# Performance work log

Hardware: AMD Instinct MI355X
Metric: run time of the kernel (lower is better)

Reference implementation:

```python
import jax, jax.numpy as jnp
import numpy as np
from jax import lax

DIM = 192
HEADS = 6
WIDTH = 256
HEIGHT = 128
BATCH = 2


def _conv1x1(x, w):
    # x: [b,c,h,w], w: [o,c] (1x1 conv, no bias)
    return jnp.einsum('bchw,oc->bohw', x, w)


def setup_inputs() -> dict:
    key = jax.random.key(0)
    ks = jax.random.split(key, 7)
    c = DIM
    std = c ** -0.5
    x = jax.random.normal(ks[0], (BATCH, c, HEIGHT, WIDTH), dtype=jnp.float32)
    rpb_table = 0.02 * jax.random.normal(ks[1], (2 * WIDTH - 1, HEADS), dtype=jnp.float32)
    w_qkv = std * jax.random.normal(ks[2], (3 * c, c), dtype=jnp.float32)
    w_depth = (1.0 / 3.0) * jax.random.normal(ks[3], (3 * c, 1, 3, 3), dtype=jnp.float32)
    w_pre = std * jax.random.normal(ks[4], (c, c), dtype=jnp.float32)
    w_out = std * jax.random.normal(ks[5], (c, c), dtype=jnp.float32)
    w_gate = std * jax.random.normal(ks[6], (c, c), dtype=jnp.float32)
    return {"x": x, "rpb_table": rpb_table, "w_qkv": w_qkv, "w_depth": w_depth,
            "w_pre": w_pre, "w_out": w_out, "w_gate": w_gate, "num_heads": HEADS}


def reference(x, rpb_table, w_qkv, w_depth, w_pre, w_out, w_gate, num_heads):
    b, c, h, w = x.shape
    hd = c // num_heads
    scale = hd ** -0.5

    x_gate = jax.nn.silu(_conv1x1(x, w_gate))

    t = _conv1x1(x, w_qkv)  # [b, 3c, h, w]
    qkv = lax.conv_general_dilated(
        t, w_depth, window_strides=(1, 1), padding='SAME',
        feature_group_count=3 * c,
        dimension_numbers=('NCHW', 'OIHW', 'NCHW'))
    q, k, v = jnp.split(qkv, 3, axis=1)

    def _rows(z):
        # 'b (head c) h w -> b h head w c'
        return z.reshape(b, num_heads, hd, h, w).transpose(0, 3, 1, 4, 2)

    q = _rows(q) * scale
    k = _rows(k)
    v = _rows(v)

    attn = jnp.einsum('bhnic,bhnjc->bhnij', q, k)  # [b, h, heads, w, w]

    # relative position bias: index[i, j] = i - j + (w - 1)
    idx = jnp.arange(w)[:, None] - jnp.arange(w)[None, :] + (w - 1)
    bias = rpb_table[idx].transpose(2, 0, 1)  # [heads, w, w]
    attn = jax.nn.softmax(attn + bias[None, None], axis=-1)

    out = jnp.einsum('bhnij,bhnjc->bhnic', attn, v)
    # 'b h head w c -> b (head c) h w'
    out = out.transpose(0, 2, 4, 1, 3).reshape(b, c, h, w)

    out = _conv1x1(out, w_pre) * x_gate
    return _conv1x1(out, w_out)
```

## Files before the change

kernel.cpp:

```cpp
#include <hip/hip_runtime.h>
#include <hip/hip_bf16.h>
#include <math.h>

#define BATCH 2
#define C 192
#define H 128
#define W 256
#define HEADS 6
#define HD 32
#define HW (H * W)
#define C3 (3 * C)
#define NPX (BATCH * HW)

typedef unsigned short ushort_t;
using bf16x8 = __attribute__((ext_vector_type(8))) short;
using f32x4  = __attribute__((ext_vector_type(4))) float;

static __device__ __forceinline__ float bfbits2f(ushort_t u) {
    return __uint_as_float(((unsigned)u) << 16);
}
static __device__ __forceinline__ ushort_t f2bfbits(float f) {
    __hip_bfloat16 h = __float2bfloat16(f);
    return *reinterpret_cast<ushort_t*>(&h);
}

__global__ __launch_bounds__(256) void prep_w_kernel(
    const float* __restrict__ wq, const float* __restrict__ wg,
    const float* __restrict__ wp, const float* __restrict__ wo,
    ushort_t* __restrict__ dst)
{
    const int i = blockIdx.x * 256 + threadIdx.x;
    const float* src; int off, base;
    if (i < 27648)      { src = wq; off = i;         base = 0; }
    else if (i < 36864) { src = wg; off = i - 27648; base = 110592; }
    else if (i < 46080) { src = wp; off = i - 36864; base = 147456; }
    else                { src = wo; off = i - 46080; base = 184320; }
    float4 v = ((const float4*)src)[off];
    if (i < 9216) {
        const float sc = 0.25503488f;
        v.x *= sc; v.y *= sc; v.z *= sc; v.w *= sc;
    }
    ushort4 o;
    o.x = f2bfbits(v.x); o.y = f2bfbits(v.y);
    o.z = f2bfbits(v.z); o.w = f2bfbits(v.w);
    *(ushort4*)(dst + base + off * 4) = o;
}

__global__ __launch_bounds__(256) void transpose_x_kernel(
    const float* __restrict__ x, ushort_t* __restrict__ xt)
{
    __shared__ uint Xs[64 * 97];
    const int p0 = blockIdx.x * 64;
    const int b  = p0 >> 15, hw0 = p0 & (HW - 1);
    const int t  = threadIdx.x;

    {
        const int px = t & 63, g = t >> 6;
        const float* xb = x + (size_t)b * C * HW + hw0 + px;
#pragma unroll
        for (int i = 0; i < 24; ++i) {
            const int cp = g + i * 4;
            const float v0 = xb[(size_t)(2 * cp) * HW];
            const float v1 = xb[(size_t)(2 * cp + 1) * HW];
            Xs[px * 97 + cp] = (uint)f2bfbits(v0) | ((uint)f2bfbits(v1) << 16);
        }
    }
    __syncthreads();
    {
        const int px = t >> 2, grp = t & 3;
        uint* dst = (uint*)(xt + (size_t)(p0 + px) * C) + grp * 24;
        const uint* s = &Xs[px * 97 + grp * 24];
#pragma unroll
        for (int i = 0; i < 6; ++i) {
            uint4 u;
            u.x = s[i * 4 + 0]; u.y = s[i * 4 + 1];
            u.z = s[i * 4 + 2]; u.w = s[i * 4 + 3];
            *(uint4*)(dst + i * 4) = u;
        }
    }
}

template <int MODE, int OUTKIND, int MT>
__global__ __launch_bounds__(256, 2) void conv_mfma_kernel(
    const ushort_t* __restrict__ in_t, const ushort_t* __restrict__ w_bf,
    void* __restrict__ outp, ushort_t* __restrict__ gate, int ostride)
{
    const int lin = blockIdx.x;
    const int xcd = lin & 7;
    const int jj  = lin >> 3;
    const int pin = jj / MT;
    const int m   = jj - pin * MT;
    const int m0  = m * 64;
    const int p0  = (xcd * 32 + pin) * 256;

    const int t  = threadIdx.x;
    const int wv = t >> 6, lane = t & 63, quad = lane >> 4, l16 = lane & 15;

    __shared__ ushort_t smem[18432];
    ushort_t* As = smem;

    const ushort_t* bp = in_t + (size_t)(p0 + wv * 64 + l16) * C + quad * 8;
    bf16x8 bF[6][4];
#pragma unroll
    for (int ks = 0; ks < 6; ++ks)
#pragma unroll
        for (int ct = 0; ct < 4; ++ct)
            bF[ks][ct] = *(const bf16x8*)(bp + (size_t)(ct * 16) * C + ks * 32);

    {
        const int row = t >> 2, cg = (t & 3) * 48;
        const ushort_t* src = w_bf + (size_t)(m0 + row) * C + cg;
        ushort_t* dst = &As[row * 200 + cg];
#pragma unroll
        for (int i = 0; i < 6; ++i)
            *(bf16x8*)(dst + i * 8) = *(const bf16x8*)(src + i * 8);
    }
    __syncthreads();

    f32x4 acc[4][4];
#pragma unroll
    for (int rt = 0; rt < 4; ++rt)
#pragma unroll
        for (int ct = 0; ct < 4; ++ct) acc[rt][ct] = f32x4{0.f, 0.f, 0.f, 0.f};

#pragma unroll
    for (int ks = 0; ks < 6; ++ks) {
        bf16x8 aF[4];
#pragma unroll
        for (int rt = 0; rt < 4; ++rt)
            aF[rt] = *(const bf16x8*)&As[(rt * 16 + l16) * 200 + quad * 8 + ks * 32];
#pragma unroll
        for (int rt = 0; rt < 4; ++rt)
#pragma unroll
            for (int ct = 0; ct < 4; ++ct)
                acc[rt][ct] = __builtin_amdgcn_mfma_f32_16x16x32_bf16(
                    aF[rt], bF[ks][ct], acc[rt][ct], 0, 0, 0);
    }

    const bool isg = (MODE == 3) && (m >= 9);
    if (MODE == 1 || isg) {
#pragma unroll
        for (int rt = 0; rt < 4; ++rt)
#pragma unroll
            for (int ct = 0; ct < 4; ++ct) {
                f32x4 v = acc[rt][ct];
#pragma unroll
                for (int r = 0; r < 4; ++r)
                    v[r] = v[r] / (1.f + __expf(-v[r]));
                acc[rt][ct] = v;
            }
    }
    if (MODE == 2) {
#pragma unroll
        for (int rt = 0; rt < 4; ++rt)
#pragma unroll
            for (int ct = 0; ct < 4; ++ct) {
                const int px = p0 + wv * 64 + ct * 16 + l16;
                const int ch = m0 + rt * 16 + quad * 4;
                const ushort4 g = *(const ushort4*)(gate + (size_t)px * C + ch);
                f32x4 v = acc[rt][ct];
                v[0] *= bfbits2f(g.x); v[1] *= bfbits2f(g.y);
                v[2] *= bfbits2f(g.z); v[3] *= bfbits2f(g.w);
                acc[rt][ct] = v;
            }
    }

    if constexpr (OUTKIND == 0) {
        __syncthreads();
        ushort_t* Ls = smem;
#pragma unroll
        for (int rt = 0; rt < 4; ++rt)
#pragma unroll
            for (int ct = 0; ct < 4; ++ct) {
                const f32x4 v = acc[rt][ct];
                ushort4 o;
                o.x = f2bfbits(v[0]); o.y = f2bfbits(v[1]);
                o.z = f2bfbits(v[2]); o.w = f2bfbits(v[3]);
                *(ushort4*)&Ls[(wv * 64 + ct * 16 + l16) * 72 +
                               rt * 16 + quad * 4] = o;
            }
        __syncthreads();

        ushort_t* ob; int osr, chb;
        if constexpr (MODE == 3) {
            ob  = isg ? gate : (ushort_t*)outp;
            osr = isg ? C : C3;
            chb = isg ? m0 - C3 : m0;
        } else {
            ob = (ushort_t*)outp; osr = ostride; chb = m0;
        }
        const int pxl = t >> 3, c8 = (t & 7) * 8;
#pragma unroll
        for (int r = 0; r < 8; ++r) {
            const int px = r * 32 + pxl;
            const bf16x8 v = *(const bf16x8*)&Ls[px * 72 + c8];
            *(bf16x8*)(ob + (size_t)(p0 + px) * osr + chb + c8) = v;
        }
    } else {
        const int bb = p0 >> 15;
        const int hwb = (p0 & (HW - 1)) + wv * 64;
        float* ob = (float*)outp + ((size_t)bb * C + m0) * HW + hwb;
#pragma unroll
        for (int rt = 0; rt < 4; ++rt)
#pragma unroll
            for (int ct = 0; ct < 4; ++ct) {
                const f32x4 v = acc[rt][ct];
#pragma unroll
                for (int r = 0; r < 4; ++r)
                    ob[(size_t)(rt * 16 + quad * 4 + r) * HW + ct * 16 + l16] = v[r];
            }
    }
}

__global__ __launch_bounds__(256) void dwconv3x3_px_kernel(
    const ushort_t* __restrict__ tin, const float* __restrict__ wd,
    ushort_t* __restrict__ out)
{
    __shared__ float wloc[576];
    __shared__ ushort_t Ld[128 * 72];
    const int cb  = blockIdx.y;
    const int tid = threadIdx.x;
    if (tid < 144)
        *(float4*)&wloc[tid * 4] = *(const float4*)(wd + cb * 576 + tid * 4);
    __syncthreads();

    const int chloc = (tid & 7) * 8;
    const int pxl0 = (tid >> 3) * 4;
    const int px = blockIdx.x * 128 + pxl0;
    const int x0 = px & (W - 1);
    const int y  = (px >> 8) & (H - 1);

    const ushort_t* tb = tin + (size_t)px * C3 + cb * 64 + chloc;

    float acc[4][8];
#pragma unroll
    for (int i = 0; i < 4; ++i)
#pragma unroll
        for (int k = 0; k < 8; ++k) acc[i][k] = 0.f;

#pragma unroll
    for (int dy = -1; dy <= 1; ++dy) {
        const int yy = y + dy;
        if (yy < 0 || yy >= H) continue;
        const ushort_t* rp = tb + (ptrdiff_t)dy * W * C3;

        float f[6][8];
#pragma unroll
        for (int d = 0; d < 6; ++d) {
            const int xx = x0 + d - 1;
            if (xx < 0 || xx >= W) {
#pragma unroll
                for (int k = 0; k < 8; ++k) f[d][k] = 0.f;
            } else {
                const bf16x8 v = *(const bf16x8*)(rp + (ptrdiff_t)(d - 1) * C3);
#pragma unroll
                for (int k = 0; k < 8; ++k) f[d][k] = bfbits2f((ushort_t)v[k]);
            }
        }
#pragma unroll
        for (int k = 0; k < 8; ++k) {
            const float* wk = &wloc[(chloc + k) * 9 + (dy + 1) * 3];
            const float w0 = wk[0], w1 = wk[1], w2 = wk[2];
#pragma unroll
            for (int i = 0; i < 4; ++i)
                acc[i][k] += f[i][k] * w0 + f[i + 1][k] * w1 + f[i + 2][k] * w2;
        }
    }

#pragma unroll
    for (int i = 0; i < 4; ++i) {
        bf16x8 o;
#pragma unroll
        for (int k = 0; k < 8; ++k) o[k] = (short)f2bfbits(acc[i][k]);
        *(bf16x8*)&Ld[(pxl0 + i) * 72 + chloc] = o;
    }
    __syncthreads();

    const int pxl = tid >> 3, c8 = (tid & 7) * 8;
#pragma unroll
    for (int r = 0; r < 4; ++r) {
        const int p = r * 32 + pxl;
        const bf16x8 v = *(const bf16x8*)&Ld[p * 72 + c8];
        *(bf16x8*)(out + (size_t)(blockIdx.x * 128 + p) * C3 + cb * 64 + c8) = v;
    }
}

__global__ __launch_bounds__(256, 4) void attention_mfma_kernel(
    const ushort_t* __restrict__ qkv, const float* __restrict__ rpb,
    ushort_t* __restrict__ att)
{
    const int y    = blockIdx.x;
    const int head = blockIdx.y;
    const int b    = blockIdx.z;
    const int t    = threadIdx.x;
    const int wv   = t >> 6;
    const int lane = t & 63;
    const int quad = lane >> 4;
    const int l16  = lane & 15;

    __shared__ __align__(16) char smem[39424];
    ushort_t* Vt = (ushort_t*)smem;
    ushort_t* Pb = (ushort_t*)(smem + 16896);
    ushort_t* rb = (ushort_t*)(smem + 37376);
    float*    Ol = (float*)smem;

    const size_t rowbase = ((size_t)b * HW + (size_t)y * W) * C3;
    const ushort_t* qbase = qkv + rowbase + head * HD + quad * 8;
    const ushort_t* kbase = qbase + C;

    {
        const ushort_t* rowp = qkv + rowbase + (size_t)t * C3 + head * HD;
        bf16x8 vfr[4];
#pragma unroll
        for (int g = 0; g < 4; ++g)
            vfr[g] = *(const bf16x8*)(rowp + 2 * C + g * 8);
#pragma unroll
        for (int g = 0; g < 4; ++g)
#pragma unroll
            for (int k = 0; k < 8; ++k)
                Vt[(g * 8 + k) * 264 + t] = (ushort_t)vfr[g][k];
    }
    {
        const float LOG2E = 1.4426950408889634f;
#pragma unroll
        for (int s2 = 0; s2 < 2; ++s2)
#pragma unroll
            for (int pp = 0; pp < 2; ++pp) {
                const int k = pp * 256 + t;
                const int src = k + s2;
                rb[s2 * 512 + k] =
                    f2bfbits(src <= 510 ? rpb[src * HEADS + head] * LOG2E : 0.f);
            }
    }

    bf16x8 aQ[4];
#pragma unroll
    for (int rt = 0; rt < 4; ++rt)
        aQ[rt] = *(const bf16x8*)(qbase + (size_t)(wv * 64 + rt * 16 + l16) * C3);
    bf16x8 bK = *(const bf16x8*)(kbase + (size_t)l16 * C3);

    __syncthreads();

    ushort_t* PbW = Pb + wv * 2560;
    float lsum[4] = {0.f, 0.f, 0.f, 0.f};
    f32x4 o_acc[4][2];
#pragma unroll
    for (int rt = 0; rt < 4; ++rt)
#pragma unroll
        for (int ct = 0; ct < 2; ++ct)
            o_acc[rt][ct] = f32x4{0.f, 0.f, 0.f, 0.f};

    const int ibase = wv * 64 + l16 + 255 - quad * 4;

    for (int c2 = 0; c2 < 8; ++c2) {
#pragma unroll
        for (int half = 0; half < 2; ++half) {
            const int n  = c2 * 2 + half;
            const int nn = (n < 15) ? n + 1 : 15;
            const bf16x8 bKn =
                *(const bf16x8*)(kbase + (size_t)(nn * 16 + l16) * C3);
#pragma unroll
            for (int rt = 0; rt < 4; ++rt) {
                const int a  = ibase + rt * 16 - n * 16 - 3;
                const int s2 = a & 1;
                const uint* tp = (const uint*)(rb + s2 * 512 + (a - s2));
                const uint u0 = tp[0], u1 = tp[1];
                f32x4 s;
                s[0] = __uint_as_float(u1 & 0xffff0000u);
                s[1] = __uint_as_float(u1 << 16);
                s[2] = __uint_as_float(u0 & 0xffff0000u);
                s[3] = __uint_as_float(u0 << 16);
                s = __builtin_amdgcn_mfma_f32_16x16x32_bf16(bK, aQ[rt], s, 0, 0, 0);
                const float p0 = __builtin_amdgcn_exp2f(s[0]);
                const float p1 = __builtin_amdgcn_exp2f(s[1]);
                const float p2 = __builtin_amdgcn_exp2f(s[2]);
                const float p3 = __builtin_amdgcn_exp2f(s[3]);
                lsum[rt] += (p0 + p1) + (p2 + p3);
                uint2 dd;
                dd.x = (uint)f2bfbits(p0) | ((uint)f2bfbits(p1) << 16);
                dd.y = (uint)f2bfbits(p2) | ((uint)f2bfbits(p3) << 16);
                *(uint2*)&PbW[(rt * 16 + l16) * 40 + half * 16 + quad * 4] = dd;
            }
            bK = bKn;
        }
#pragma unroll
        for (int rt = 0; rt < 4; ++rt) {
            const bf16x8 aP = *(const bf16x8*)&PbW[(rt * 16 + l16) * 40 + quad * 8];
#pragma unroll
            for (int ct = 0; ct < 2; ++ct) {
                const bf16x8 bV = *(const bf16x8*)
                    &Vt[(ct * 16 + l16) * 264 + c2 * 32 + quad * 8];
                o_acc[rt][ct] = __builtin_amdgcn_mfma_f32_16x16x32_bf16(
                    aP, bV, o_acc[rt][ct], 0, 0, 0);
            }
        }
    }

    float linv[4];
#pragma unroll
    for (int rt = 0; rt < 4; ++rt) {
        float v = lsum[rt];
        v += __shfl_xor(v, 16);
        v += __shfl_xor(v, 32);
        linv[rt] = 1.f / v;
    }

    __syncthreads();
#pragma unroll
    for (int rt = 0; rt < 4; ++rt) {
        const int i = wv * 64 + rt * 16 + quad * 4;
        float sc[4];
#pragma unroll
        for (int reg = 0; reg < 4; ++reg)
            sc[reg] = __shfl(linv[rt], quad * 4 + reg);
#pragma unroll
        for (int ct = 0; ct < 2; ++ct) {
            const int c = ct * 16 + l16;
#pragma unroll
            for (int reg = 0; reg < 4; ++reg)
                Ol[c * 257 + i + reg] = o_acc[rt][ct][reg] * sc[reg];
        }
    }
    __syncthreads();

    const size_t orow = (size_t)b * HW + (size_t)y * W;
    const int pxl = t >> 2, part = t & 3;
#pragma unroll
    for (int r = 0; r < 4; ++r) {
        const int px = r * 64 + pxl;
        bf16x8 o;
#pragma unroll
        for (int k = 0; k < 8; ++k)
            o[k] = (short)f2bfbits(Ol[(part * 8 + k) * 257 + px]);
        *(bf16x8*)(att + (orow + px) * C + head * HD + part * 8) = o;
    }
}

extern "C" void kernel_launch(void* const* d_in, const int* in_sizes, int n_in,
                              void* d_out, int out_size, void* d_ws, size_t ws_size,
                              hipStream_t stream)
{
    const float* x       = (const float*)d_in[0];
    const float* rpb     = (const float*)d_in[1];
    const float* w_qkv   = (const float*)d_in[2];
    const float* w_depth = (const float*)d_in[3];
    const float* w_pre   = (const float*)d_in[4];
    const float* w_out   = (const float*)d_in[5];
    const float* w_gate  = (const float*)d_in[6];
    float* out = (float*)d_out;

    char* wsb = (char*)d_ws;
    ushort_t* wbf      = (ushort_t*)wsb;
    ushort_t* w_pre_b  = wbf + 147456;
    ushort_t* w_out_b  = wbf + 184320;
    ushort_t* gate_t   = (ushort_t*)(wsb + 524288u);
    ushort_t* buf_t    = (ushort_t*)(wsb + 25690112u);
    ushort_t* att_t    = (ushort_t*)(wsb + 25690112u);
    ushort_t* y_t      = (ushort_t*)(wsb + 50855936u);
    ushort_t* buf_qkv  = (ushort_t*)(wsb + 101187584u);
    ushort_t* x_t      = (ushort_t*)(wsb + 101187584u);

    dim3 blk(256);

    prep_w_kernel<<<dim3(216), blk, 0, stream>>>(w_qkv, w_gate, w_pre, w_out, wbf);
    transpose_x_kernel<<<dim3(NPX / 64), blk, 0, stream>>>(x, x_t);
    conv_mfma_kernel<3, 0, 12><<<dim3(3072), blk, 0, stream>>>(
        x_t, wbf, buf_t, gate_t, C3);
    dwconv3x3_px_kernel<<<dim3(NPX / 128, 9), blk, 0, stream>>>(
        buf_t, w_depth, buf_qkv);
    attention_mfma_kernel<<<dim3(H, HEADS, BATCH), blk, 0, stream>>>(
        buf_qkv, rpb, att_t);
    conv_mfma_kernel<2, 0, 3><<<dim3(768), blk, 0, stream>>>(
        att_t, w_pre_b, y_t, gate_t, C);
    conv_mfma_kernel<0, 1, 3><<<dim3(768), blk, 0, stream>>>(
        y_t, w_out_b, out, nullptr, C);
}
```

Measured before the change: 284.4 us.

## Fuse pre and out projections with gating; remap blocks for XCD locality

```diff
diff --git a/kernel.cpp b/kernel.cpp
--- a/kernel.cpp
+++ b/kernel.cpp
@@ -150,20 +150,6 @@
                 acc[rt][ct] = v;
             }
     }
-    if (MODE == 2) {
-#pragma unroll
-        for (int rt = 0; rt < 4; ++rt)
-#pragma unroll
-            for (int ct = 0; ct < 4; ++ct) {
-                const int px = p0 + wv * 64 + ct * 16 + l16;
-                const int ch = m0 + rt * 16 + quad * 4;
-                const ushort4 g = *(const ushort4*)(gate + (size_t)px * C + ch);
-                f32x4 v = acc[rt][ct];
-                v[0] *= bfbits2f(g.x); v[1] *= bfbits2f(g.y);
-                v[2] *= bfbits2f(g.z); v[3] *= bfbits2f(g.w);
-                acc[rt][ct] = v;
-            }
-    }
 
     if constexpr (OUTKIND == 0) {
         __syncthreads();
@@ -218,6 +204,8 @@
 {
     __shared__ float wloc[576];
     __shared__ ushort_t Ld[128 * 72];
+    const int bx = blockIdx.x;
+    const int px_blk = (bx & 7) * 64 + (63 - (bx >> 3));
     const int cb  = blockIdx.y;
     const int tid = threadIdx.x;
     if (tid < 144)
@@ -226,7 +214,7 @@
 
     const int chloc = (tid & 7) * 8;
     const int pxl0 = (tid >> 3) * 4;
-    const int px = blockIdx.x * 128 + pxl0;
+    const int px = px_blk * 128 + pxl0;
     const int x0 = px & (W - 1);
     const int y  = (px >> 8) & (H - 1);
 
@@ -281,7 +269,7 @@
     for (int r = 0; r < 4; ++r) {
         const int p = r * 32 + pxl;
         const bf16x8 v = *(const bf16x8*)&Ld[p * 72 + c8];
-        *(bf16x8*)(out + (size_t)(blockIdx.x * 128 + p) * C3 + cb * 64 + c8) = v;
+        *(bf16x8*)(out + (size_t)(px_blk * 128 + p) * C3 + cb * 64 + c8) = v;
     }
 }
 
@@ -289,9 +277,12 @@
     const ushort_t* __restrict__ qkv, const float* __restrict__ rpb,
     ushort_t* __restrict__ att)
 {
-    const int y    = blockIdx.x;
-    const int head = blockIdx.y;
-    const int b    = blockIdx.z;
+    const int lin  = blockIdx.x;
+    const int xcd  = lin & 7;
+    const int j    = lin >> 3;
+    const int b    = xcd >> 2;
+    const int y    = (xcd & 3) * 32 + (j & 31);
+    const int head = j >> 5;
     const int t    = threadIdx.x;
     const int wv   = t >> 6;
     const int lane = t & 63;
@@ -436,6 +427,107 @@
     }
 }
 
+__global__ __launch_bounds__(256, 3) void conv2_fused_kernel(
+    const ushort_t* __restrict__ att_t, const ushort_t* __restrict__ gatep,
+    const ushort_t* __restrict__ wpre, const ushort_t* __restrict__ wout,
+    float* __restrict__ outp)
+{
+    const int lin = blockIdx.x;
+    const int xcd = lin & 7;
+    const int pin = lin >> 3;
+    const int p0  = (xcd * 64 + pin) * 128;
+
+    const int t  = threadIdx.x;
+    const int wv = t >> 6, lane = t & 63, quad = lane >> 4, l16 = lane & 15;
+
+    __shared__ ushort_t Zs[4][32 * 200];
+    ushort_t* Zw = Zs[wv];
+    const int pxw = p0 + wv * 32;
+
+#pragma unroll
+    for (int ms = 0; ms < 3; ++ms) {
+        f32x4 acc[4][2];
+#pragma unroll
+        for (int rt = 0; rt < 4; ++rt)
+#pragma unroll
+            for (int ct = 0; ct < 2; ++ct) acc[rt][ct] = f32x4{0.f,0.f,0.f,0.f};
+
+        const ushort_t* ap = wpre + (size_t)(ms * 64 + l16) * C + quad * 8;
+        const ushort_t* bp = att_t + (size_t)(pxw + l16) * C + quad * 8;
+#pragma unroll
+        for (int ks = 0; ks < 6; ++ks) {
+            bf16x8 aF[4];
+#pragma unroll
+            for (int rt = 0; rt < 4; ++rt)
+                aF[rt] = *(const bf16x8*)(ap + (size_t)(rt * 16) * C + ks * 32);
+            const bf16x8 b0 = *(const bf16x8*)(bp + ks * 32);
+            const bf16x8 b1 = *(const bf16x8*)(bp + (size_t)16 * C + ks * 32);
+#pragma unroll
+            for (int rt = 0; rt < 4; ++rt) {
+                acc[rt][0] = __builtin_amdgcn_mfma_f32_16x16x32_bf16(
+                    aF[rt], b0, acc[rt][0], 0, 0, 0);
+                acc[rt][1] = __builtin_amdgcn_mfma_f32_16x16x32_bf16(
+                    aF[rt], b1, acc[rt][1], 0, 0, 0);
+            }
+        }
+#pragma unroll
+        for (int rt = 0; rt < 4; ++rt)
+#pragma unroll
+            for (int ct = 0; ct < 2; ++ct) {
+                const int px = pxw + ct * 16 + l16;
+                const int ch = ms * 64 + rt * 16 + quad * 4;
+                const ushort4 g = *(const ushort4*)(gatep + (size_t)px * C + ch);
+                f32x4 v = acc[rt][ct];
+                v[0] *= bfbits2f(g.x); v[1] *= bfbits2f(g.y);
+                v[2] *= bfbits2f(g.z); v[3] *= bfbits2f(g.w);
+                ushort4 o;
+                o.x = f2bfbits(v[0]); o.y = f2bfbits(v[1]);
+                o.z = f2bfbits(v[2]); o.w = f2bfbits(v[3]);
+                *(ushort4*)&Zw[(ct * 16 + l16) * 200 + ch] = o;
+            }
+    }
+
+    const int bb  = p0 >> 15;
+    const int hwb = (p0 & (HW - 1)) + wv * 32;
+#pragma unroll
+    for (int ms = 0; ms < 3; ++ms) {
+        f32x4 acc[4][2];
+#pragma unroll
+        for (int rt = 0; rt < 4; ++rt)
+#pragma unroll
+            for (int ct = 0; ct < 2; ++ct) acc[rt][ct] = f32x4{0.f,0.f,0.f,0.f};
+
+        const ushort_t* ap = wout + (size_t)(ms * 64 + l16) * C + quad * 8;
+#pragma unroll
+        for (int ks = 0; ks < 6; ++ks) {
+            bf16x8 aF[4];
+#pragma unroll
+            for (int rt = 0; rt < 4; ++rt)
+                aF[rt] = *(const bf16x8*)(ap + (size_t)(rt * 16) * C + ks * 32);
+            const bf16x8 b0 = *(const bf16x8*)&Zw[l16 * 200 + quad * 8 + ks * 32];
+            const bf16x8 b1 = *(const bf16x8*)&Zw[(16 + l16) * 200 + quad * 8 + ks * 32];
+#pragma unroll
+            for (int rt = 0; rt < 4; ++rt) {
+                acc[rt][0] = __builtin_amdgcn_mfma_f32_16x16x32_bf16(
+                    aF[rt], b0, acc[rt][0], 0, 0, 0);
+                acc[rt][1] = __builtin_amdgcn_mfma_f32_16x16x32_bf16(
+                    aF[rt], b1, acc[rt][1], 0, 0, 0);
+            }
+        }
+        float* ob = outp + ((size_t)bb * C + ms * 64) * HW + hwb;
+#pragma unroll
+        for (int rt = 0; rt < 4; ++rt)
+#pragma unroll
+            for (int ct = 0; ct < 2; ++ct) {
+                const f32x4 v = acc[rt][ct];
+#pragma unroll
+                for (int r = 0; r < 4; ++r)
+                    __builtin_nontemporal_store(v[r],
+                        &ob[(size_t)(rt * 16 + quad * 4 + r) * HW + ct * 16 + l16]);
+            }
+    }
+}
+
 extern "C" void kernel_launch(void* const* d_in, const int* in_sizes, int n_in,
                               void* d_out, int out_size, void* d_ws, size_t ws_size,
                               hipStream_t stream)
@@ -456,7 +548,6 @@
     ushort_t* gate_t   = (ushort_t*)(wsb + 524288u);
     ushort_t* buf_t    = (ushort_t*)(wsb + 25690112u);
     ushort_t* att_t    = (ushort_t*)(wsb + 25690112u);
-    ushort_t* y_t      = (ushort_t*)(wsb + 50855936u);
     ushort_t* buf_qkv  = (ushort_t*)(wsb + 101187584u);
     ushort_t* x_t      = (ushort_t*)(wsb + 101187584u);
 
@@ -468,10 +559,8 @@
         x_t, wbf, buf_t, gate_t, C3);
     dwconv3x3_px_kernel<<<dim3(NPX / 128, 9), blk, 0, stream>>>(
         buf_t, w_depth, buf_qkv);
-    attention_mfma_kernel<<<dim3(H, HEADS, BATCH), blk, 0, stream>>>(
+    attention_mfma_kernel<<<dim3(H * HEADS * BATCH), blk, 0, stream>>>(
         buf_qkv, rpb, att_t);
-    conv_mfma_kernel<2, 0, 3><<<dim3(768), blk, 0, stream>>>(
-        att_t, w_pre_b, y_t, gate_t, C);
-    conv_mfma_kernel<0, 1, 3><<<dim3(768), blk, 0, stream>>>(
-        y_t, w_out_b, out, nullptr, C);
-}
+    conv2_fused_kernel<<<dim3(NPX / 128), blk, 0, stream>>>(
+        att_t, gate_t, w_pre_b, w_out_b, out);
+}
```

Measured after the change: 285.6 us. No clear change (+0.4%).
